# Optimization experiments

Measured on AMD Instinct MI355X. Metric: run time of the kernel, lower is better.

Reference implementation:

```python
import jax, jax.numpy as jnp
import numpy as np
import math

B, S, D, H = 4, 1024, 512, 8
DK = D // H
NEG = -1e32


def setup_inputs() -> dict:
    key = jax.random.key(0)
    ks = jax.random.split(key, 16)
    f = lambda k, shape: jax.random.normal(k, shape, dtype=jnp.float32)
    w = 1.0 / math.sqrt(D)  # xavier-ish scale
    return {
        'query_mean': f(ks[0], (B, S, D)),
        'query_cov': f(ks[1], (B, S, D)),
        'key_mean': f(ks[2], (B, S, D)),
        'key_cov': f(ks[3], (B, S, D)),
        'values_mean': f(ks[4], (B, S, D)),
        'values_cov': f(ks[5], (B, S, D)),
        'Wk_mean': f(ks[6], (D, D)) * w, 'bk_mean': jnp.zeros((D,), jnp.float32),
        'Wk_cov': f(ks[7], (D, D)) * w, 'bk_cov': jnp.zeros((D,), jnp.float32),
        'Wv_mean': f(ks[8], (D, D)) * w, 'bv_mean': jnp.zeros((D,), jnp.float32),
        'Wv_cov': f(ks[9], (D, D)) * w, 'bv_cov': jnp.zeros((D,), jnp.float32),
        'Wo_mean': f(ks[10], (D, D)) * w, 'bo_mean': jnp.zeros((D,), jnp.float32),
        'Wo_cov': f(ks[11], (D, D)) * w, 'bo_cov': jnp.zeros((D,), jnp.float32),
        'gammas': f(ks[12], (H, 1, 1)) * 0.1,
        'mask': jnp.tril(jnp.ones((1, 1, S, S), dtype=jnp.int32)),
    }


def _forward(query_mean, query_cov, key_mean, key_cov, values_mean, values_cov,
             Wk_mean, bk_mean, Wk_cov, bk_cov, Wv_mean, bv_mean, Wv_cov, bv_cov,
             Wo_mean, bo_mean, Wo_cov, bo_cov, gammas, mask):
    def heads(x, W, b):  # [B,S,D] -> [B,H,S,DK]
        return (x @ W + b).reshape(B, S, H, DK).transpose(0, 2, 1, 3)

    # kq_same=True: queries and keys share the k linears
    qm = heads(query_mean, Wk_mean, bk_mean)
    qc = heads(query_cov, Wk_cov, bk_cov)
    km = heads(key_mean, Wk_mean, bk_mean)
    kc = heads(key_cov, Wk_cov, bk_cov)
    vm = heads(values_mean, Wv_mean, bv_mean)
    vc = heads(values_cov, Wv_cov, bv_cov)

    inv = 1.0 / math.sqrt(DK)
    sm = jnp.einsum('bhqd,bhkd->bhqk', qm, km) * inv  # [B,H,S,S]
    sc = jnp.einsum('bhqd,bhkd->bhqk', qc, kc) * inv

    maskf = mask.astype(jnp.float32)
    # position_effect[i,j] = |j - i|
    pos = jnp.abs(jnp.arange(S)[None, :] - jnp.arange(S)[:, None]).astype(jnp.float32)[None, None]

    def dist_scores(s):
        p = jax.nn.softmax(jnp.where(mask == 0, NEG, s), axis=-1) * maskf
        cum = jnp.cumsum(p, axis=-1)
        tot = jnp.sum(p, axis=-1, keepdims=True)
        return jnp.sqrt(jnp.clip((tot - cum) * pos, 0.0, None))

    dm = jax.lax.stop_gradient(dist_scores(sm))  # torch no_grad + detach
    dc = jax.lax.stop_gradient(dist_scores(sc))

    gv = -jax.nn.softplus(gammas)[None]  # [1,H,1,1]
    em = jnp.clip(jnp.exp(dm * gv), 1e-5, 1e5)
    ec = jnp.clip(jnp.exp(dc * gv), 1e-5, 1e5)

    am = jax.nn.softmax(jnp.where(mask == 0, NEG, sm * em), axis=-1)
    ac = jax.nn.softmax(jnp.where(mask == 0, NEG, sc * ec), axis=-1)

    om = jnp.einsum('bhqk,bhkd->bhqd', am, vm).transpose(0, 2, 1, 3).reshape(B, S, D)
    oc = jnp.einsum('bhqk,bhkd->bhqd', ac, vc).transpose(0, 2, 1, 3).reshape(B, S, D)
    return om @ Wo_mean + bo_mean, oc @ Wo_cov + bo_cov


def reference(query_mean, query_cov, key_mean, key_cov, values_mean, values_cov,
              Wk_mean, bk_mean, Wk_cov, bk_cov, Wv_mean, bv_mean, Wv_cov, bv_cov,
              Wo_mean, bo_mean, Wo_cov, bo_cov, gammas, mask):
    return _forward(query_mean, query_cov, key_mean, key_cov, values_mean, values_cov,
                    Wk_mean, bk_mean, Wk_cov, bk_cov, Wv_mean, bv_mean, Wv_cov, bv_cov,
                    Wo_mean, bo_mean, Wo_cov, bo_cov, gammas, mask)
```

## Files before the change

### kernel.cpp

```cpp
#include <hip/hip_runtime.h>
#include <hip/hip_bf16.h>
#include <math.h>

constexpr int B_  = 4;
constexpr int S_  = 1024;
constexpr int D_  = 512;
constexpr int H_  = 8;
constexpr int DK_ = 64;
constexpr int MROWS_ = B_ * S_;
constexpr size_t SZ_ = (size_t)B_ * H_ * S_ * DK_;
constexpr size_t WSZ_ = (size_t)D_ * D_;

typedef __attribute__((ext_vector_type(8))) short bf16x8;
typedef __attribute__((ext_vector_type(4))) float f32x4;

__device__ __forceinline__ float bf2f(unsigned short u) {
  union { unsigned int u; float f; } v; v.u = (unsigned int)u << 16; return v.f;
}
__device__ __forceinline__ unsigned short f2bf(float f) {
  union { float f; unsigned int u; } v; v.f = f;
  unsigned int r = v.u + 0x7FFFu + ((v.u >> 16) & 1u);
  return (unsigned short)(r >> 16);
}

template <int CTRL>
__device__ __forceinline__ float dpp_mov_f(float x) {
  return __builtin_bit_cast(float,
      __builtin_amdgcn_update_dpp(0, __builtin_bit_cast(int, x), CTRL, 0xF, 0xF, true));
}
__device__ __forceinline__ float scan16(float v) {
  v += dpp_mov_f<0x111>(v);
  v += dpp_mov_f<0x112>(v);
  v += dpp_mov_f<0x114>(v);
  v += dpp_mov_f<0x118>(v);
  return v;
}
__device__ __forceinline__ float red16(float v) {
  v += dpp_mov_f<0x128>(v);
  v += dpp_mov_f<0x124>(v);
  v += dpp_mov_f<0x122>(v);
  v += dpp_mov_f<0x121>(v);
  return v;
}
__device__ __forceinline__ float bcast15(float v) {
  return __builtin_bit_cast(float,
      __builtin_amdgcn_ds_swizzle(__builtin_bit_cast(int, v), 0x01F0));
}

struct TpArgs { const float* W[4]; unsigned short* out[4]; };

__global__ __launch_bounds__(256) void wtrans(TpArgs a) {
  const int z = blockIdx.z;
  const float* __restrict__ W = a.W[z];
  unsigned short* __restrict__ out = a.out[z];
  __shared__ float T[64][65];
  const int tid = threadIdx.x;
  const int tx = blockIdx.x & 7, ty = blockIdx.x >> 3;
  const int k0 = ty * 64, n0 = tx * 64;
#pragma unroll
  for (int i = 0; i < 4; ++i) {
    const int idx = tid + i * 256;
    const int r = idx >> 4, c4 = (idx & 15) * 4;
    const float4 w = *(const float4*)&W[(size_t)(k0 + r) * D_ + n0 + c4];
    T[r][c4 + 0] = w.x; T[r][c4 + 1] = w.y; T[r][c4 + 2] = w.z; T[r][c4 + 3] = w.w;
  }
  __syncthreads();
#pragma unroll
  for (int i = 0; i < 4; ++i) {
    const int idx = tid + i * 256;
    const int n = idx >> 4, kc = (idx & 15) * 4;
    ushort4 pk;
    pk.x = f2bf(T[kc + 0][n]); pk.y = f2bf(T[kc + 1][n]);
    pk.z = f2bf(T[kc + 2][n]); pk.w = f2bf(T[kc + 3][n]);
    *(ushort4*)&out[(size_t)(n0 + n) * D_ + k0 + kc] = pk;
  }
}

struct ProjArgs {
  const float* A[6]; const unsigned short* Wt[6]; const float* bias[6];
  unsigned short* out[6]; int vmode[6];
};

__global__ __launch_bounds__(256) void proj_mfma(ProjArgs args) {
  const int z = blockIdx.z;
  const float* __restrict__ A = args.A[z];
  const unsigned short* __restrict__ Wt = args.Wt[z];
  const float* __restrict__ bias = args.bias[z];
  unsigned short* __restrict__ out = args.out[z];
  const int vmode = args.vmode[z];

  __shared__ unsigned short Abuf[128][40];
  __shared__ unsigned short Bbuf[128][40];
  const int tid = threadIdx.x, wv = tid >> 6, lane = tid & 63;
  const int quad = lane >> 4, l16 = lane & 15;
  const int wm = wv >> 1, wn = wv & 1;
  const int n0 = blockIdx.x * 128, m0 = blockIdx.y * 128;

  f32x4 acc[4][4];
#pragma unroll
  for (int i = 0; i < 4; ++i)
#pragma unroll
    for (int j = 0; j < 4; ++j) acc[i][j] = (f32x4){0.f, 0.f, 0.f, 0.f};

  for (int kt = 0; kt < 16; ++kt) {
    const int k0 = kt * 32;
    __syncthreads();
#pragma unroll
    for (int i = 0; i < 4; ++i) {
      const int idx = tid + i * 256;
      const int m = idx >> 3, c = idx & 7;
      const float4 av = *(const float4*)&A[(size_t)(m0 + m) * D_ + k0 + c * 4];
      ushort4 p;
      p.x = f2bf(av.x); p.y = f2bf(av.y); p.z = f2bf(av.z); p.w = f2bf(av.w);
      *(ushort4*)&Abuf[m][c * 4] = p;
    }
#pragma unroll
    for (int i = 0; i < 2; ++i) {
      const int idx = tid + i * 256;
      const int n = idx >> 2, c = idx & 3;
      *(uint4*)&Bbuf[n][c * 8] = *(const uint4*)&Wt[(size_t)(n0 + n) * D_ + k0 + c * 8];
    }
    __syncthreads();

    bf16x8 af[4], bfr[4];
#pragma unroll
    for (int i = 0; i < 4; ++i) af[i] = *(const bf16x8*)&Abuf[wm * 64 + i * 16 + l16][quad * 8];
#pragma unroll
    for (int j = 0; j < 4; ++j) bfr[j] = *(const bf16x8*)&Bbuf[wn * 64 + j * 16 + l16][quad * 8];
#pragma unroll
    for (int i = 0; i < 4; ++i)
#pragma unroll
      for (int j = 0; j < 4; ++j)
        acc[i][j] = __builtin_amdgcn_mfma_f32_16x16x32_bf16(af[i], bfr[j], acc[i][j], 0, 0, 0);
  }

#pragma unroll
  for (int j = 0; j < 4; ++j) {
    const int col = n0 + wn * 64 + j * 16 + l16;
    const float bv = bias[col];
    const int h = col >> 6, dk = col & 63;
#pragma unroll
    for (int i = 0; i < 4; ++i) {
      const int mbase = m0 + wm * 64 + i * 16 + quad * 4;
      const int b = mbase >> 10;
      if (!vmode) {
#pragma unroll
        for (int r = 0; r < 4; ++r) {
          const int s = (mbase + r) & 1023;
          out[(((size_t)b * H_ + h) * S_ + s) * DK_ + dk] = f2bf(acc[i][j][r] + bv);
        }
      } else {
        const int s = mbase & 1023;
        ushort4 pk;
        pk.x = f2bf(acc[i][j][0] + bv); pk.y = f2bf(acc[i][j][1] + bv);
        pk.z = f2bf(acc[i][j][2] + bv); pk.w = f2bf(acc[i][j][3] + bv);
        *(ushort4*)&out[(((size_t)b * H_ + h) * DK_ + dk) * S_ + s] = pk;
      }
    }
  }
}

struct OutArgs {
  const unsigned short* A[2]; const unsigned short* Wt[2];
  const float* bias[2]; float* out[2];
};

__global__ __launch_bounds__(256) void out_mfma(OutArgs args) {
  const int z = blockIdx.z;
  const unsigned short* __restrict__ A = args.A[z];
  const unsigned short* __restrict__ Wt = args.Wt[z];
  const float* __restrict__ bias = args.bias[z];
  float* __restrict__ out = args.out[z];

  __shared__ unsigned short Abuf[128][40];
  __shared__ unsigned short Bbuf[128][40];
  const int tid = threadIdx.x, wv = tid >> 6, lane = tid & 63;
  const int quad = lane >> 4, l16 = lane & 15;
  const int wm = wv >> 1, wn = wv & 1;
  const int n0 = blockIdx.x * 128, m0 = blockIdx.y * 128;

  f32x4 acc[4][4];
#pragma unroll
  for (int i = 0; i < 4; ++i)
#pragma unroll
    for (int j = 0; j < 4; ++j) acc[i][j] = (f32x4){0.f, 0.f, 0.f, 0.f};

  for (int kt = 0; kt < 16; ++kt) {
    const int k0 = kt * 32;
    __syncthreads();
#pragma unroll
    for (int i = 0; i < 2; ++i) {
      const int idx = tid + i * 256;
      const int m = idx >> 2, c = idx & 3;
      *(uint4*)&Abuf[m][c * 8] = *(const uint4*)&A[(size_t)(m0 + m) * D_ + k0 + c * 8];
    }
#pragma unroll
    for (int i = 0; i < 2; ++i) {
      const int idx = tid + i * 256;
      const int n = idx >> 2, c = idx & 3;
      *(uint4*)&Bbuf[n][c * 8] = *(const uint4*)&Wt[(size_t)(n0 + n) * D_ + k0 + c * 8];
    }
    __syncthreads();

    bf16x8 af[4], bfr[4];
#pragma unroll
    for (int i = 0; i < 4; ++i) af[i] = *(const bf16x8*)&Abuf[wm * 64 + i * 16 + l16][quad * 8];
#pragma unroll
    for (int j = 0; j < 4; ++j) bfr[j] = *(const bf16x8*)&Bbuf[wn * 64 + j * 16 + l16][quad * 8];
#pragma unroll
    for (int i = 0; i < 4; ++i)
#pragma unroll
      for (int j = 0; j < 4; ++j)
        acc[i][j] = __builtin_amdgcn_mfma_f32_16x16x32_bf16(af[i], bfr[j], acc[i][j], 0, 0, 0);
  }

#pragma unroll
  for (int j = 0; j < 4; ++j) {
    const int col = n0 + wn * 64 + j * 16 + l16;
    const float bv = bias[col];
#pragma unroll
    for (int i = 0; i < 4; ++i) {
      const int mbase = m0 + wm * 64 + i * 16 + quad * 4;
#pragma unroll
      for (int r = 0; r < 4; ++r)
        out[(size_t)(mbase + r) * D_ + col] = acc[i][j][r] + bv;
    }
  }
}

__global__ __launch_bounds__(512) void attn_mfma(
    const unsigned short* __restrict__ qkv, const float* __restrict__ gammas,
    unsigned short* __restrict__ Obase)
{
  __shared__ unsigned short Ps[8][16][72];

  const int tid = threadIdx.x;
  const int w = tid >> 6, lane = tid & 63, quad = lane >> 4, l16 = lane & 15;
  const int bh = blockIdx.x;
  const int pair = blockIdx.y;
  const int ch = blockIdx.z;
  const int qt = (w < 4) ? (15 - pair) : pair;
  const int wq = w & 3;
  const int q0 = qt << 6;
  const int b = bh >> 3, h = bh & 7;

  const unsigned short* Q  = qkv + (size_t)ch * 3 * SZ_ + (size_t)bh * S_ * DK_;
  const unsigned short* K  = qkv + (size_t)ch * 3 * SZ_ + SZ_ + (size_t)bh * S_ * DK_;
  const unsigned short* Vt = qkv + (size_t)ch * 3 * SZ_ + 2 * SZ_ + (size_t)bh * (size_t)DK_ * S_;
  unsigned short* O = Obase + (size_t)ch * SZ_;

  const float g = gammas[h];
  const float gv = -(fmaxf(g, 0.f) + log1pf(__expf(-fabsf(g))));

  const unsigned short* Qrow = Q + (size_t)(q0 + wq * 16 + l16) * DK_;
  const bf16x8 qf0 = *(const bf16x8*)(Qrow + quad * 8);
  const bf16x8 qf1 = *(const bf16x8*)(Qrow + 32 + quad * 8);
  const int myrow = q0 + wq * 16 + quad * 4;

  float Tacc[4] = {0.f, 0.f, 0.f, 0.f};
  for (int kt = 0; kt <= qt; ++kt) {
    f32x4 sa[4];
#pragma unroll
    for (int cb = 0; cb < 4; ++cb) {
      const unsigned short* Kr = K + (size_t)(kt * 64 + cb * 16 + l16) * DK_;
      const bf16x8 kf0 = *(const bf16x8*)(Kr + quad * 8);
      const bf16x8 kf1 = *(const bf16x8*)(Kr + 32 + quad * 8);
      f32x4 a = {0.f, 0.f, 0.f, 0.f};
      a = __builtin_amdgcn_mfma_f32_16x16x32_bf16(qf0, kf0, a, 0, 0, 0);
      a = __builtin_amdgcn_mfma_f32_16x16x32_bf16(qf1, kf1, a, 0, 0, 0);
      sa[cb] = a;
    }
    if (kt == qt) {
#pragma unroll
      for (int cb = 0; cb < 4; ++cb)
#pragma unroll
        for (int r = 0; r < 4; ++r) {
          float e = __expf(sa[cb][r] * 0.125f);
          if ((kt * 64 + cb * 16 + l16) > (myrow + r)) e = 0.f;
          Tacc[r] += e;
        }
    } else {
#pragma unroll
      for (int cb = 0; cb < 4; ++cb)
#pragma unroll
        for (int r = 0; r < 4; ++r)
          Tacc[r] += __expf(sa[cb][r] * 0.125f);
    }
  }
  float invT[4];
#pragma unroll
  for (int r = 0; r < 4; ++r) invT[r] = 1.f / red16(Tacc[r]);

  float carry[4] = {0.f, 0.f, 0.f, 0.f};
  float l2a[4] = {0.f, 0.f, 0.f, 0.f};
  f32x4 oacc[4];
#pragma unroll
  for (int cb = 0; cb < 4; ++cb) oacc[cb] = (f32x4){0.f, 0.f, 0.f, 0.f};

  for (int kt = 0; kt <= qt; ++kt) {
    bf16x8 vf0[4], vf1[4];
#pragma unroll
    for (int cb = 0; cb < 4; ++cb) {
      const unsigned short* Vr = Vt + (size_t)(cb * 16 + l16) * S_ + kt * 64;
      vf0[cb] = *(const bf16x8*)(Vr + quad * 8);
      vf1[cb] = *(const bf16x8*)(Vr + 32 + quad * 8);
    }

    f32x4 sa[4];
#pragma unroll
    for (int cb = 0; cb < 4; ++cb) {
      const unsigned short* Kr = K + (size_t)(kt * 64 + cb * 16 + l16) * DK_;
      const bf16x8 kf0 = *(const bf16x8*)(Kr + quad * 8);
      const bf16x8 kf1 = *(const bf16x8*)(Kr + 32 + quad * 8);
      f32x4 a = {0.f, 0.f, 0.f, 0.f};
      a = __builtin_amdgcn_mfma_f32_16x16x32_bf16(qf0, kf0, a, 0, 0, 0);
      a = __builtin_amdgcn_mfma_f32_16x16x32_bf16(qf1, kf1, a, 0, 0, 0);
      sa[cb] = a;
    }
#pragma unroll
    for (int cb = 0; cb < 4; ++cb)
#pragma unroll
      for (int r = 0; r < 4; ++r) sa[cb][r] *= 0.125f;
    if (kt == qt) {
#pragma unroll
      for (int cb = 0; cb < 4; ++cb)
#pragma unroll
        for (int r = 0; r < 4; ++r)
          if ((kt * 64 + cb * 16 + l16) > (myrow + r)) sa[cb][r] = -1e30f;
    }

#pragma unroll
    for (int r = 0; r < 4; ++r) {
      float v0 = scan16(__expf(sa[0][r]));
      float v1 = scan16(__expf(sa[1][r]));
      float v2 = scan16(__expf(sa[2][r]));
      float v3 = scan16(__expf(sa[3][r]));
      const float tt0 = bcast15(v0), tt1 = bcast15(v1);
      const float tt2 = bcast15(v2), tt3 = bcast15(v3);
      const float base = carry[r];
      const float p01 = tt0 + tt1, p012 = p01 + tt2;
      const float cum0 = (base + v0) * invT[r];
      const float cum1 = (base + tt0 + v1) * invT[r];
      const float cum2 = (base + p01 + v2) * invT[r];
      const float cum3 = (base + p012 + v3) * invT[r];
      carry[r] = base + p012 + tt3;

      const float bpos = (float)(myrow + r) - (float)(kt * 64 + l16);
      float st0, st1, st2, st3;
      {
        float dd = sqrtf(fmaxf((1.f - cum0) * bpos, 0.f));
        st0 = sa[0][r] * fminf(fmaxf(__expf(dd * gv), 1e-5f), 1e5f);
        dd = sqrtf(fmaxf((1.f - cum1) * (bpos - 16.f), 0.f));
        st1 = sa[1][r] * fminf(fmaxf(__expf(dd * gv), 1e-5f), 1e5f);
        dd = sqrtf(fmaxf((1.f - cum2) * (bpos - 32.f), 0.f));
        st2 = sa[2][r] * fminf(fmaxf(__expf(dd * gv), 1e-5f), 1e5f);
        dd = sqrtf(fmaxf((1.f - cum3) * (bpos - 48.f), 0.f));
        st3 = sa[3][r] * fminf(fmaxf(__expf(dd * gv), 1e-5f), 1e5f);
      }

      const float w0 = __expf(st0), w1 = __expf(st1);
      const float w2 = __expf(st2), w3 = __expf(st3);
      l2a[r] += (w0 + w1) + (w2 + w3);
      const int prow = quad * 4 + r;
      Ps[w][prow][ 0 + l16] = f2bf(w0);
      Ps[w][prow][16 + l16] = f2bf(w1);
      Ps[w][prow][32 + l16] = f2bf(w2);
      Ps[w][prow][48 + l16] = f2bf(w3);
    }
    asm volatile("s_waitcnt lgkmcnt(0)" ::: "memory");

    const bf16x8 pf0 = *(const bf16x8*)&Ps[w][l16][quad * 8];
    const bf16x8 pf1 = *(const bf16x8*)&Ps[w][l16][32 + quad * 8];
#pragma unroll
    for (int cb = 0; cb < 4; ++cb) {
      oacc[cb] = __builtin_amdgcn_mfma_f32_16x16x32_bf16(pf0, vf0[cb], oacc[cb], 0, 0, 0);
      oacc[cb] = __builtin_amdgcn_mfma_f32_16x16x32_bf16(pf1, vf1[cb], oacc[cb], 0, 0, 0);
    }
  }

#pragma unroll
  for (int r = 0; r < 4; ++r) {
    const float inv = 1.f / red16(l2a[r]);
    const int srow = myrow + r;
    const size_t base = ((size_t)b * S_ + srow) * D_ + h * DK_;
    O[base +  0 + l16] = f2bf(oacc[0][r] * inv);
    O[base + 16 + l16] = f2bf(oacc[1][r] * inv);
    O[base + 32 + l16] = f2bf(oacc[2][r] * inv);
    O[base + 48 + l16] = f2bf(oacc[3][r] * inv);
  }
}

extern "C" void kernel_launch(void* const* d_in, const int* in_sizes, int n_in,
                              void* d_out, int out_size, void* d_ws, size_t ws_size,
                              hipStream_t stream) {
  const float* query_mean  = (const float*)d_in[0];
  const float* query_cov   = (const float*)d_in[1];
  const float* key_mean    = (const float*)d_in[2];
  const float* key_cov     = (const float*)d_in[3];
  const float* values_mean = (const float*)d_in[4];
  const float* values_cov  = (const float*)d_in[5];
  const float* Wk_mean = (const float*)d_in[6];
  const float* bk_mean = (const float*)d_in[7];
  const float* Wk_cov  = (const float*)d_in[8];
  const float* bk_cov  = (const float*)d_in[9];
  const float* Wv_mean = (const float*)d_in[10];
  const float* bv_mean = (const float*)d_in[11];
  const float* Wv_cov  = (const float*)d_in[12];
  const float* bv_cov  = (const float*)d_in[13];
  const float* Wo_mean = (const float*)d_in[14];
  const float* bo_mean = (const float*)d_in[15];
  const float* Wo_cov  = (const float*)d_in[16];
  const float* bo_cov  = (const float*)d_in[17];
  const float* gammas  = (const float*)d_in[18];

  unsigned short* qkv  = (unsigned short*)d_ws;
  unsigned short* obuf = qkv + 6 * SZ_;
  unsigned short* Wt4  = (unsigned short*)d_out;
  unsigned short* Wot  = qkv + 2 * SZ_;
  float* out = (float*)d_out;

  TpArgs t1;
  t1.W[0] = Wk_mean; t1.W[1] = Wv_mean; t1.W[2] = Wk_cov; t1.W[3] = Wv_cov;
  for (int i = 0; i < 4; ++i) t1.out[i] = Wt4 + (size_t)i * WSZ_;
  wtrans<<<dim3(64, 1, 4), 256, 0, stream>>>(t1);

  ProjArgs pa;
  const float* pA[6] = {query_mean, key_mean, values_mean, query_cov, key_cov, values_cov};
  const int   wIdx[6] = {0, 0, 1, 2, 2, 3};
  const float* pb[6] = {bk_mean, bk_mean, bv_mean, bk_cov, bk_cov, bv_cov};
  const int pv[6] = {0, 0, 1, 0, 0, 1};
  for (int i = 0; i < 6; ++i) {
    pa.A[i] = pA[i]; pa.Wt[i] = Wt4 + (size_t)wIdx[i] * WSZ_; pa.bias[i] = pb[i];
    pa.out[i] = qkv + (size_t)i * SZ_; pa.vmode[i] = pv[i];
  }
  proj_mfma<<<dim3(4, 32, 6), 256, 0, stream>>>(pa);

  attn_mfma<<<dim3(32, 8, 2), 512, 0, stream>>>(qkv, gammas, obuf);

  TpArgs t2;
  t2.W[0] = Wo_mean; t2.W[1] = Wo_cov; t2.W[2] = Wo_mean; t2.W[3] = Wo_cov;
  t2.out[0] = Wot; t2.out[1] = Wot + WSZ_; t2.out[2] = Wot; t2.out[3] = Wot + WSZ_;
  wtrans<<<dim3(64, 1, 2), 256, 0, stream>>>(t2);

  OutArgs oa;
  oa.A[0] = obuf;        oa.A[1] = obuf + SZ_;
  oa.Wt[0] = Wot;        oa.Wt[1] = Wot + WSZ_;
  oa.bias[0] = bo_mean;  oa.bias[1] = bo_cov;
  oa.out[0] = out;       oa.out[1] = out + (size_t)MROWS_ * D_;
  out_mfma<<<dim3(4, 32, 2), 256, 0, stream>>>(oa);
}
```

Before: 272.0 us.

## Split attention blocks per query tile and use exp2 with folded log2e scaling

The attention kernel no longer pairs a heavy and a light query tile in one 512-thread block. It launches one 256-thread block per query tile, ordered heaviest first, so the scheduler does the load balancing with smaller blocks. The 1/sqrt(dk) scale and the gamma factor are pre-multiplied by log2(e), so every exponential becomes a bare exp2 with no extra multiply. The bf16 packing of P also switches to a cheaper round-half-up conversion. The risks are worse load balance or tail behaviour without pairing, and slightly different rounding in P.

After: 289.1 us. +6.3%, slower.

```diff
diff --git a/kernel.cpp b/kernel.cpp
--- a/kernel.cpp
+++ b/kernel.cpp
@@ -21,6 +21,10 @@
   union { float f; unsigned int u; } v; v.f = f;
   unsigned int r = v.u + 0x7FFFu + ((v.u >> 16) & 1u);
   return (unsigned short)(r >> 16);
+}
+__device__ __forceinline__ unsigned short f2bf_ru(float f) {
+  union { float f; unsigned int u; } v; v.f = f;
+  return (unsigned short)((v.u + 0x8000u) >> 16);
 }
 
 template <int CTRL>
@@ -228,21 +232,23 @@
   }
 }
 
-__global__ __launch_bounds__(512) void attn_mfma(
+__global__ __launch_bounds__(256) void attn_mfma(
     const unsigned short* __restrict__ qkv, const float* __restrict__ gammas,
     unsigned short* __restrict__ Obase)
 {
-  __shared__ unsigned short Ps[8][16][72];
+  __shared__ unsigned short Ps[4][16][72];
 
   const int tid = threadIdx.x;
   const int w = tid >> 6, lane = tid & 63, quad = lane >> 4, l16 = lane & 15;
   const int bh = blockIdx.x;
-  const int pair = blockIdx.y;
+  const int qt = 15 - (int)blockIdx.y;
   const int ch = blockIdx.z;
-  const int qt = (w < 4) ? (15 - pair) : pair;
-  const int wq = w & 3;
+  const int wq = w;
   const int q0 = qt << 6;
   const int b = bh >> 3, h = bh & 7;
+
+  constexpr float SC_ = 0.125f * 1.4426950408889634f;
+  constexpr float LOG2E_ = 1.4426950408889634f;
 
   const unsigned short* Q  = qkv + (size_t)ch * 3 * SZ_ + (size_t)bh * S_ * DK_;
   const unsigned short* K  = qkv + (size_t)ch * 3 * SZ_ + SZ_ + (size_t)bh * S_ * DK_;
@@ -250,7 +256,7 @@
   unsigned short* O = Obase + (size_t)ch * SZ_;
 
   const float g = gammas[h];
-  const float gv = -(fmaxf(g, 0.f) + log1pf(__expf(-fabsf(g))));
+  const float gv2 = -(fmaxf(g, 0.f) + log1pf(__expf(-fabsf(g)))) * LOG2E_;
 
   const unsigned short* Qrow = Q + (size_t)(q0 + wq * 16 + l16) * DK_;
   const bf16x8 qf0 = *(const bf16x8*)(Qrow + quad * 8);
@@ -275,7 +281,7 @@
       for (int cb = 0; cb < 4; ++cb)
 #pragma unroll
         for (int r = 0; r < 4; ++r) {
-          float e = __expf(sa[cb][r] * 0.125f);
+          float e = exp2f(sa[cb][r] * SC_);
           if ((kt * 64 + cb * 16 + l16) > (myrow + r)) e = 0.f;
           Tacc[r] += e;
         }
@@ -284,7 +290,7 @@
       for (int cb = 0; cb < 4; ++cb)
 #pragma unroll
         for (int r = 0; r < 4; ++r)
-          Tacc[r] += __expf(sa[cb][r] * 0.125f);
+          Tacc[r] += exp2f(sa[cb][r] * SC_);
     }
   }
   float invT[4];
@@ -320,7 +326,7 @@
 #pragma unroll
     for (int cb = 0; cb < 4; ++cb)
 #pragma unroll
-      for (int r = 0; r < 4; ++r) sa[cb][r] *= 0.125f;
+      for (int r = 0; r < 4; ++r) sa[cb][r] *= SC_;
     if (kt == qt) {
 #pragma unroll
       for (int cb = 0; cb < 4; ++cb)
@@ -331,10 +337,10 @@
 
 #pragma unroll
     for (int r = 0; r < 4; ++r) {
-      float v0 = scan16(__expf(sa[0][r]));
-      float v1 = scan16(__expf(sa[1][r]));
-      float v2 = scan16(__expf(sa[2][r]));
-      float v3 = scan16(__expf(sa[3][r]));
+      float v0 = scan16(exp2f(sa[0][r]));
+      float v1 = scan16(exp2f(sa[1][r]));
+      float v2 = scan16(exp2f(sa[2][r]));
+      float v3 = scan16(exp2f(sa[3][r]));
       const float tt0 = bcast15(v0), tt1 = bcast15(v1);
       const float tt2 = bcast15(v2), tt3 = bcast15(v3);
       const float base = carry[r];
@@ -349,23 +355,23 @@
       float st0, st1, st2, st3;
       {
         float dd = sqrtf(fmaxf((1.f - cum0) * bpos, 0.f));
-        st0 = sa[0][r] * fminf(fmaxf(__expf(dd * gv), 1e-5f), 1e5f);
+        st0 = sa[0][r] * fminf(fmaxf(exp2f(dd * gv2), 1e-5f), 1e5f);
         dd = sqrtf(fmaxf((1.f - cum1) * (bpos - 16.f), 0.f));
-        st1 = sa[1][r] * fminf(fmaxf(__expf(dd * gv), 1e-5f), 1e5f);
+        st1 = sa[1][r] * fminf(fmaxf(exp2f(dd * gv2), 1e-5f), 1e5f);
         dd = sqrtf(fmaxf((1.f - cum2) * (bpos - 32.f), 0.f));
-        st2 = sa[2][r] * fminf(fmaxf(__expf(dd * gv), 1e-5f), 1e5f);
+        st2 = sa[2][r] * fminf(fmaxf(exp2f(dd * gv2), 1e-5f), 1e5f);
         dd = sqrtf(fmaxf((1.f - cum3) * (bpos - 48.f), 0.f));
-        st3 = sa[3][r] * fminf(fmaxf(__expf(dd * gv), 1e-5f), 1e5f);
+        st3 = sa[3][r] * fminf(fmaxf(exp2f(dd * gv2), 1e-5f), 1e5f);
       }
 
-      const float w0 = __expf(st0), w1 = __expf(st1);
-      const float w2 = __expf(st2), w3 = __expf(st3);
+      const float w0 = exp2f(st0), w1 = exp2f(st1);
+      const float w2 = exp2f(st2), w3 = exp2f(st3);
       l2a[r] += (w0 + w1) + (w2 + w3);
       const int prow = quad * 4 + r;
-      Ps[w][prow][ 0 + l16] = f2bf(w0);
-      Ps[w][prow][16 + l16] = f2bf(w1);
-      Ps[w][prow][32 + l16] = f2bf(w2);
-      Ps[w][prow][48 + l16] = f2bf(w3);
+      Ps[w][prow][ 0 + l16] = f2bf_ru(w0);
+      Ps[w][prow][16 + l16] = f2bf_ru(w1);
+      Ps[w][prow][32 + l16] = f2bf_ru(w2);
+      Ps[w][prow][48 + l16] = f2bf_ru(w3);
     }
     asm volatile("s_waitcnt lgkmcnt(0)" ::: "memory");
 
@@ -435,7 +441,7 @@
   }
   proj_mfma<<<dim3(4, 32, 6), 256, 0, stream>>>(pa);
 
-  attn_mfma<<<dim3(32, 8, 2), 512, 0, stream>>>(qkv, gammas, obuf);
+  attn_mfma<<<dim3(32, 16, 2), 256, 0, stream>>>(qkv, gammas, obuf);
 
   TpArgs t2;
   t2.W[0] = Wo_mean; t2.W[1] = Wo_cov; t2.W[2] = Wo_mean; t2.W[3] = Wo_cov;
```
